# Kernel optimization log

Hardware: AMD Instinct MI355X
Metric: run time of the kernel (lower is better)

## Reference

```python
import jax, jax.numpy as jnp
import numpy as np

B, N, D, H, P = 4, 512, 256, 8, 3
HD = D // H
EPS = 1e-5

def _ln(x, g, b):
    m = jnp.mean(x, axis=-1, keepdims=True)
    v = jnp.var(x, axis=-1, keepdims=True)
    return (x - m) * jax.lax.rsqrt(v + EPS) * g + b

def setup_inputs() -> dict:
    key = jax.random.key(0)
    ks = jax.random.split(key, 12)
    s = lambda *sh: 1.0 / np.sqrt(sh[0])
    return {
        "x": jax.random.normal(ks[0], (B, N, D), jnp.float32),
        "mask": jax.random.randint(ks[1], (B, N), 0, 2).astype(bool),
        "pair_feat": jax.random.normal(ks[2], (B, N, N, P), jnp.float32),
        "Wqkv": jax.random.normal(ks[3], (D, 3 * D), jnp.float32) * s(D),
        "Wout": jax.random.normal(ks[4], (D, D), jnp.float32) * s(D),
        "bout": jnp.zeros((D,), jnp.float32),
        "Wp1": jax.random.normal(ks[5], (P, D), jnp.float32) * s(P),
        "bp1": jnp.zeros((D,), jnp.float32),
        "Wp2": jax.random.normal(ks[6], (D, H), jnp.float32) * s(D),
        "bp2": jnp.zeros((H,), jnp.float32),
        "Wf1": jax.random.normal(ks[7], (D, 4 * D), jnp.float32) * s(D),
        "bf1": jnp.zeros((4 * D,), jnp.float32),
        "Wf2": jax.random.normal(ks[8], (4 * D, D), jnp.float32) * s(4 * D),
        "bf2": jnp.zeros((D,), jnp.float32),
        "g1": jnp.ones((D,), jnp.float32), "b1": jnp.zeros((D,), jnp.float32),
        "g2": jnp.ones((D,), jnp.float32), "b2": jnp.zeros((D,), jnp.float32),
    }

def reference(x, mask, pair_feat, Wqkv, Wout, bout, Wp1, bp1, Wp2, bp2,
              Wf1, bf1, Wf2, bf2, g1, b1, g2, b2):
    b_, n_, d_ = x.shape
    scale = HD ** -0.5
    qkv = x @ Wqkv                                  # [B,N,3D]
    q, k, v = jnp.split(qkv, 3, axis=-1)
    q = q.reshape(b_, n_, H, HD)
    k = k.reshape(b_, n_, H, HD)
    v = v.reshape(b_, n_, H, HD)
    logits = jnp.einsum('bihd,bjhd->bhij', q, k) * scale
    # pairwise bias MLP -> per-head bias [B,H,N,N]
    bias = jax.nn.relu(pair_feat @ Wp1 + bp1) @ Wp2 + bp2   # [B,N,N,H]
    logits = logits + jnp.transpose(bias, (0, 3, 1, 2))
    key_mask = ~mask[:, None, None, :]               # [B,1,1,N]
    logits = jnp.where(key_mask, -1e9, logits)
    attn = jax.nn.softmax(logits, axis=-1)
    out = jnp.einsum('bhij,bjhd->bihd', attn, v).reshape(b_, n_, d_)
    out = out @ Wout + bout
    x = _ln(x + out, g1, b1)
    h = jax.nn.gelu(x @ Wf1 + bf1, approximate=False) @ Wf2 + bf2
    return _ln(x + h, g2, b2)
```

## Files before the change

kernel.cpp:

```cpp
#include <hip/hip_runtime.h>
#include <hip/hip_fp16.h>
#include <math.h>

typedef unsigned short u16;
typedef short s16x8 __attribute__((ext_vector_type(8)));
typedef _Float16 f16x8 __attribute__((ext_vector_type(8)));
typedef float f32x4 __attribute__((ext_vector_type(4)));
typedef unsigned int u32x2 __attribute__((ext_vector_type(2)));

constexpr int CB = 4, CN = 512, CD = 256, CH = 8, CHD = 32;
constexpr float CEPS = 1e-5f;
constexpr int M_ROWS = CB * CN;
constexpr float QSCALE = 0.17677669529663687f;

constexpr size_t O_XB    = 0;
constexpr size_t O_QB    = 1048576;
constexpr size_t O_KB    = 2097152;
constexpr size_t O_VB    = 3145728;
constexpr size_t O_WQKVT = 4194304;
constexpr size_t O_WOUTT = O_WQKVT + 393216;
constexpr size_t O_WF1T  = O_WOUTT + 131072;
constexpr size_t O_WF2T  = O_WF1T + 524288;
constexpr size_t O_WP2T  = O_WF2T + 524288;
constexpr size_t O_PACKED= O_WP2T + 8192;
constexpr size_t O_JIDX  = O_PACKED + 4096;
constexpr size_t O_BIAS  = O_JIDX + 8192;
constexpr size_t O_AOUT  = O_BIAS + 16777216;
constexpr size_t O_H1B   = O_AOUT + 1048576;
constexpr size_t O_PRE1  = O_H1B + 4194304;
constexpr size_t O_PRE2  = O_PRE1 + 2097152;
constexpr size_t O_CNT   = O_PRE2 + 2097152;

__device__ inline u16 f2b(float f) {
  union { float f; unsigned u; } v{f};
  return (u16)((v.u + 0x7FFFu + ((v.u >> 16) & 1u)) >> 16);
}
__device__ inline float b2f(u16 b) {
  union { unsigned u; float f; } v{(unsigned)b << 16};
  return v.f;
}
__device__ inline f32x4 MFMA(s16x8 a, s16x8 b, f32x4 c) {
  return __builtin_amdgcn_mfma_f32_16x16x32_bf16(a, b, c, 0, 0, 0);
}
__device__ inline f32x4 MFMAH(f16x8 a, f16x8 b, f32x4 c) {
  return __builtin_amdgcn_mfma_f32_16x16x32_f16(a, b, c, 0, 0, 0);
}
__device__ inline unsigned cvtpk(float lo, float hi) {
  unsigned r;
  asm("v_cvt_pk_bf16_f32 %0, %1, %2" : "=v"(r) : "v"(lo), "v"(hi));
  return r;
}
__device__ inline unsigned pkmax0(unsigned a) {
  unsigned d;
  asm("v_pk_max_f16 %0, %1, 0" : "=v"(d) : "v"(a));
  return d;
}

__global__ __launch_bounds__(256) void prep_kernel(
    const float* __restrict__ x, const float* __restrict__ Wqkv,
    const float* __restrict__ Wout, const float* __restrict__ Wf1,
    const float* __restrict__ Wf2, const float* __restrict__ Wp2,
    const float* __restrict__ Wp1, const float* __restrict__ bp1,
    const unsigned char* __restrict__ maskraw,
    u16* __restrict__ xb, u16* __restrict__ wqkvt, u16* __restrict__ woutt,
    u16* __restrict__ wf1t, u16* __restrict__ wf2t, u16* __restrict__ wp2t,
    unsigned* __restrict__ packed, int* __restrict__ jidxg,
    int* __restrict__ cntg) {
  __shared__ int mode_max;
  __shared__ int mdec[2048];
  int blk = blockIdx.x, tid = threadIdx.x;
  if (blk < 256) {
    for (int t = tid; t < 512; t += 256) {
      float4 v = ((const float4*)x)[blk * 512 + t];
      u16 o0 = f2b(v.x), o1 = f2b(v.y), o2 = f2b(v.z), o3 = f2b(v.w);
      u32x2 w; w.x = (unsigned)o0 | ((unsigned)o1 << 16);
      w.y = (unsigned)o2 | ((unsigned)o3 << 16);
      *(u32x2*)(xb + (size_t)(blk * 512 + t) * 4) = w;
    }
  } else if (blk < 352) {
    int o0 = (blk - 256) * 2048;
    for (int t = tid; t < 2048; t += 256) {
      int o = o0 + t, n = o >> 8, k = o & 255;
      wqkvt[o] = f2b(Wqkv[k * 768 + n]);
    }
  } else if (blk < 384) {
    int o0 = (blk - 352) * 2048;
    for (int t = tid; t < 2048; t += 256) {
      int o = o0 + t, n = o >> 8, k = o & 255;
      woutt[o] = f2b(Wout[k * 256 + n]);
    }
  } else if (blk < 512) {
    int o0 = (blk - 384) * 2048;
    for (int t = tid; t < 2048; t += 256) {
      int o = o0 + t, n = o >> 8, k = o & 255;
      wf1t[o] = f2b(Wf1[k * 1024 + n]);
    }
  } else if (blk < 640) {
    int o0 = (blk - 512) * 2048;
    for (int t = tid; t < 2048; t += 256) {
      int o = o0 + t, n = o >> 10, k = o & 1023;
      wf2t[o] = f2b(Wf2[k * 256 + n]);
    }
  } else if (blk == 640) {
    for (int t = tid; t < 4096; t += 256) {
      int h = t >> 8, c = t & 255;
      wp2t[t] = (h < 8) ? __half_as_ushort(__float2half(Wp2[c * 8 + h])) : (u16)0;
    }
    if (tid < 128) {
      int p = tid * 2;
      unsigned w0 = (unsigned)__half_as_ushort(__float2half(Wp1[p]))
                  | ((unsigned)__half_as_ushort(__float2half(Wp1[p + 1])) << 16);
      unsigned w1 = (unsigned)__half_as_ushort(__float2half(Wp1[256 + p]))
                  | ((unsigned)__half_as_ushort(__float2half(Wp1[256 + p + 1])) << 16);
      unsigned w2 = (unsigned)__half_as_ushort(__float2half(Wp1[512 + p]))
                  | ((unsigned)__half_as_ushort(__float2half(Wp1[512 + p + 1])) << 16);
      unsigned bb = (unsigned)__half_as_ushort(__float2half(bp1[p]))
                  | ((unsigned)__half_as_ushort(__float2half(bp1[p + 1])) << 16);
      uint4 o; o.x = w0; o.y = w1; o.z = w2; o.w = bb;
      ((uint4*)packed)[tid] = o;
    }
  } else {
    if (tid == 0) mode_max = 0;
    __syncthreads();
    int lm = 0;
    for (int i = tid; i < CB*CN; i += 256)
      if ((i & 3) != 0) lm = max(lm, (int)maskraw[i]);
    atomicMax(&mode_max, lm);
    __syncthreads();
    int mv = mode_max;
    for (int i = tid; i < CB*CN; i += 256) {
      int val;
      if (mv == 0)      val = (((const int*)maskraw)[i] != 0);
      else if (mv == 1) val = (maskraw[i] != 0);
      else              val = (((const unsigned int*)maskraw)[i] != 0);
      mdec[i] = val;
    }
    __syncthreads();
    int w = tid >> 6, lane = tid & 63;
    if (w < 4) {
      int b = w, basei = 0;
      for (int c = 0; c < 8; ++c) {
        int j = c * 64 + lane;
        int m = mdec[b * 512 + j];
        unsigned long long bal = __ballot(m != 0);
        int off = __popcll(bal & ((1ull << lane) - 1ull));
        if (m) jidxg[b * 512 + basei + off] = j;
        basei += (int)__popcll(bal);
      }
      if (lane == 0) cntg[b] = basei;
      for (int p = basei + lane; p < 512; p += 64) jidxg[b * 512 + p] = 0;
    }
  }
}

__global__ __launch_bounds__(256) void qkv_pbias_kernel(
    const u16* __restrict__ A, const u16* __restrict__ Wt,
    u16* __restrict__ qb, u16* __restrict__ kb, u16* __restrict__ vb,
    const float* __restrict__ pf, const unsigned* __restrict__ packed,
    const u16* __restrict__ wp2t, const float* __restrict__ bp2,
    const int* __restrict__ jidxg, const int* __restrict__ cntg,
    u16* __restrict__ biasc) {
  __shared__ uint4 smem[1024];
  const int blk = blockIdx.x, tid = threadIdx.x;
  const int lane = tid & 63, w = tid >> 6;
  if (blk < 384) {
    u16* As = (u16*)smem;
    u16* Bs = (u16*)smem + 64 * 64;
    const int wm = w >> 1, wn = w & 1;
    const int bm = (blk / 12) * 64, bn = (blk % 12) * 64;
    f32x4 fz = {0.f, 0.f, 0.f, 0.f};
    f32x4 acc[2][2] = {{fz, fz}, {fz, fz}};
    for (int k0 = 0; k0 < 256; k0 += 64) {
#pragma unroll
      for (int t = tid; t < 512; t += 256) {
        int r = t >> 3, s = t & 7;
        s16x8 v = *(const s16x8*)(A + (size_t)(bm + r) * 256 + k0 + s * 8);
        *(s16x8*)(As + r * 64 + ((s ^ (r & 7)) << 3)) = v;
      }
#pragma unroll
      for (int t = tid; t < 512; t += 256) {
        int r = t >> 3, s = t & 7;
        s16x8 v = *(const s16x8*)(Wt + (size_t)(bn + r) * 256 + k0 + s * 8);
        *(s16x8*)(Bs + r * 64 + ((s ^ (r & 7)) << 3)) = v;
      }
      __syncthreads();
#pragma unroll
      for (int ks = 0; ks < 2; ++ks) {
        s16x8 af[2], bf[2];
#pragma unroll
        for (int mf = 0; mf < 2; ++mf) {
          int r = wm * 32 + mf * 16 + (lane & 15);
          int s = ks * 4 + (lane >> 4);
          af[mf] = *(const s16x8*)(As + r * 64 + ((s ^ (r & 7)) << 3));
        }
#pragma unroll
        for (int nf = 0; nf < 2; ++nf) {
          int r = wn * 32 + nf * 16 + (lane & 15);
          int s = ks * 4 + (lane >> 4);
          bf[nf] = *(const s16x8*)(Bs + r * 64 + ((s ^ (r & 7)) << 3));
        }
#pragma unroll
        for (int mf = 0; mf < 2; ++mf)
#pragma unroll
          for (int nf = 0; nf < 2; ++nf)
            acc[mf][nf] = MFMA(af[mf], bf[nf], acc[mf][nf]);
      }
      __syncthreads();
    }
#pragma unroll
    for (int mf = 0; mf < 2; ++mf) {
#pragma unroll
      for (int nf = 0; nf < 2; ++nf) {
#pragma unroll
        for (int r = 0; r < 4; ++r) {
          int m = bm + wm * 32 + mf * 16 + (lane >> 4) * 4 + r;
          int n = bn + wn * 32 + nf * 16 + (lane & 15);
          float v = acc[mf][nf][r];
          if (n < 256) {
            qb[(size_t)m * 256 + n] = f2b(v * QSCALE);
          } else if (n < 512) {
            kb[(size_t)m * 256 + (n - 256)] = f2b(v);
          } else {
            vb[(size_t)m * 256 + (n - 512)] = f2b(v);
          }
        }
      }
    }
  } else {
    uint4* pk = smem;
    float* pfl = (float*)(smem + 128);
    int* ji = (int*)(smem + 512);
    const int bid = blk - 384;
    const int b = bid >> 9, i = bid & 511;
    const int q = lane >> 4, hr = lane & 15;
    if (tid < 128) pk[tid] = ((const uint4*)packed)[tid];
    const float4* pfr = (const float4*)(pf + (size_t)(b * 512 + i) * 1536);
#pragma unroll
    for (int t = tid; t < 384; t += 256) ((float4*)pfl)[t] = pfr[t];
    for (int t = tid; t < 512; t += 256) ji[t] = jidxg[b * 512 + t];
    const int cnt = cntg[b];
    __syncthreads();
    __half2 f0d[8], f1d[8], f2d[8];
#pragma unroll
    for (int t = 0; t < 8; ++t) {
      if (w * 128 + t * 16 < cnt) {
        int jsrc = ji[w * 128 + t * 16 + hr];
        f0d[t] = __float2half2_rn(pfl[jsrc * 3 + 0]);
        f1d[t] = __float2half2_rn(pfl[jsrc * 3 + 1]);
        f2d[t] = __float2half2_rn(pfl[jsrc * 3 + 2]);
      }
    }
    f32x4 fz = {0.f, 0.f, 0.f, 0.f};
    f32x4 acc[8] = {fz, fz, fz, fz, fz, fz, fz, fz};
    for (int chunk = 0; chunk < 8; ++chunk) {
      f16x8 wfrag = *(const f16x8*)(wp2t + hr * 256 + chunk * 32 + q * 8);
      int pbase = chunk * 16 + q * 4;
      __half2 w0[4], w1[4], w2[4], bb[4];
#pragma unroll
      for (int p = 0; p < 4; ++p) {
        uint4 c = pk[pbase + p];
        w0[p] = *(const __half2*)&c.x;
        w1[p] = *(const __half2*)&c.y;
        w2[p] = *(const __half2*)&c.z;
        bb[p] = *(const __half2*)&c.w;
      }
#pragma unroll
      for (int t = 0; t < 8; ++t) {
        if (w * 128 + t * 16 < cnt) {
          union { unsigned u[4]; f16x8 v; } af;
#pragma unroll
          for (int p = 0; p < 4; ++p) {
            __half2 h = __hfma2(f0d[t], w0[p], bb[p]);
            h = __hfma2(f1d[t], w1[p], h);
            h = __hfma2(f2d[t], w2[p], h);
            af.u[p] = pkmax0(*(const unsigned*)&h);
          }
          acc[t] = MFMAH(af.v, wfrag, acc[t]);
        }
      }
    }
    if (hr < 8) {
      float bb = bp2[hr];
      size_t base = ((size_t)(b * 8 + hr) * 512 + i) * 512;
#pragma unroll
      for (int t = 0; t < 8; ++t) {
        if (w * 128 + t * 16 < cnt) {
          int p0 = w * 128 + t * 16 + q * 4;
          u32x2 o;
          o.x = cvtpk(acc[t][0] + bb, acc[t][1] + bb);
          o.y = cvtpk(acc[t][2] + bb, acc[t][3] + bb);
          *(u32x2*)(biasc + base + p0) = o;
        }
      }
    }
  }
}

__global__ __launch_bounds__(256) void mgemm_res(
    const u16* __restrict__ A, const u16* __restrict__ Wt,
    const float* __restrict__ bias, const float* __restrict__ R,
    float* __restrict__ outf, int N, int K) {
  __shared__ u16 As[32 * 64];
  __shared__ u16 Bs[64 * 64];
  const int tid = threadIdx.x;
  const int lane = tid & 63, w = tid >> 6;
  const int wm = w >> 1, wn = w & 1;
  const int bm = blockIdx.y * 32, bn = blockIdx.x * 64;
  f32x4 fz = {0.f, 0.f, 0.f, 0.f};
  f32x4 acc[2] = {fz, fz};
  for (int k0 = 0; k0 < K; k0 += 64) {
    for (int t = tid; t < 256; t += 256) {
      int r = t >> 3, s = t & 7;
      s16x8 v = *(const s16x8*)(A + (size_t)(bm + r) * K + k0 + s * 8);
      *(s16x8*)(As + r * 64 + ((s ^ (r & 7)) << 3)) = v;
    }
#pragma unroll
    for (int t = tid; t < 512; t += 256) {
      int r = t >> 3, s = t & 7;
      s16x8 v = *(const s16x8*)(Wt + (size_t)(bn + r) * K + k0 + s * 8);
      *(s16x8*)(Bs + r * 64 + ((s ^ (r & 7)) << 3)) = v;
    }
    __syncthreads();
#pragma unroll
    for (int ks = 0; ks < 2; ++ks) {
      int r = wm * 16 + (lane & 15);
      int s = ks * 4 + (lane >> 4);
      s16x8 af = *(const s16x8*)(As + r * 64 + ((s ^ (r & 7)) << 3));
#pragma unroll
      for (int nf = 0; nf < 2; ++nf) {
        int br = wn * 32 + nf * 16 + (lane & 15);
        s16x8 bf = *(const s16x8*)(Bs + br * 64 + ((s ^ (br & 7)) << 3));
        acc[nf] = MFMA(af, bf, acc[nf]);
      }
    }
    __syncthreads();
  }
#pragma unroll
  for (int nf = 0; nf < 2; ++nf) {
#pragma unroll
    for (int r = 0; r < 4; ++r) {
      int m = bm + wm * 16 + (lane >> 4) * 4 + r;
      int n = bn + wn * 32 + nf * 16 + (lane & 15);
      outf[(size_t)m * N + n] = acc[nf][r] + bias[n] + R[(size_t)m * N + n];
    }
  }
}

__global__ __launch_bounds__(256) void ffn1_kernel(
    const float* __restrict__ pre1, const u16* __restrict__ Wt,
    const float* __restrict__ bias, const float* __restrict__ g1,
    const float* __restrict__ b1, u16* __restrict__ outb) {
  __shared__ u16 As[64 * 64];
  __shared__ u16 Bs[64 * 64];
  __shared__ float rowm[64], rowr[64];
  const int tid = threadIdx.x;
  const int lane = tid & 63, w = tid >> 6;
  const int wm = w >> 1, wn = w & 1;
  const int bm = blockIdx.y * 64, bn = blockIdx.x * 64;
  {
    int r = tid >> 2, qd = tid & 3;
    const float4* pr = (const float4*)(pre1 + (size_t)(bm + r) * 256 + qd * 64);
    float s = 0.f, ss = 0.f;
#pragma unroll
    for (int u = 0; u < 16; ++u) {
      float4 v = pr[u];
      s += v.x + v.y + v.z + v.w;
      ss += v.x*v.x + v.y*v.y + v.z*v.z + v.w*v.w;
    }
    s += __shfl_xor(s, 1); ss += __shfl_xor(ss, 1);
    s += __shfl_xor(s, 2); ss += __shfl_xor(ss, 2);
    if (qd == 0) {
      float mean = s * (1.0f / 256.0f);
      float var  = ss * (1.0f / 256.0f) - mean * mean;
      rowm[r] = mean; rowr[r] = rsqrtf(var + CEPS);
    }
  }
  __syncthreads();
  f32x4 fz = {0.f, 0.f, 0.f, 0.f};
  f32x4 acc[2][2] = {{fz, fz}, {fz, fz}};
  for (int k0 = 0; k0 < 256; k0 += 64) {
#pragma unroll
    for (int t = tid; t < 512; t += 256) {
      int r = t >> 3, s = t & 7;
      float mean = rowm[r], rstd = rowr[r];
      const float4* pr = (const float4*)(pre1 + (size_t)(bm + r) * 256 + k0 + s * 8);
      float4 a0 = pr[0], a1 = pr[1];
      const float4* gp = (const float4*)(g1 + k0 + s * 8);
      const float4* bp = (const float4*)(b1 + k0 + s * 8);
      float4 g0 = gp[0], g1v = gp[1], c0 = bp[0], c1 = bp[1];
      union { unsigned u[4]; s16x8 v; } pk2;
      pk2.u[0] = cvtpk((a0.x-mean)*rstd*g0.x + c0.x, (a0.y-mean)*rstd*g0.y + c0.y);
      pk2.u[1] = cvtpk((a0.z-mean)*rstd*g0.z + c0.z, (a0.w-mean)*rstd*g0.w + c0.w);
      pk2.u[2] = cvtpk((a1.x-mean)*rstd*g1v.x + c1.x, (a1.y-mean)*rstd*g1v.y + c1.y);
      pk2.u[3] = cvtpk((a1.z-mean)*rstd*g1v.z + c1.z, (a1.w-mean)*rstd*g1v.w + c1.w);
      *(s16x8*)(As + r * 64 + ((s ^ (r & 7)) << 3)) = pk2.v;
    }
#pragma unroll
    for (int t = tid; t < 512; t += 256) {
      int r = t >> 3, s = t & 7;
      s16x8 v = *(const s16x8*)(Wt + (size_t)(bn + r) * 256 + k0 + s * 8);
      *(s16x8*)(Bs + r * 64 + ((s ^ (r & 7)) << 3)) = v;
    }
    __syncthreads();
#pragma unroll
    for (int ks = 0; ks < 2; ++ks) {
      s16x8 af[2], bf[2];
#pragma unroll
      for (int mf = 0; mf < 2; ++mf) {
        int r = wm * 32 + mf * 16 + (lane & 15);
        int s = ks * 4 + (lane >> 4);
        af[mf] = *(const s16x8*)(As + r * 64 + ((s ^ (r & 7)) << 3));
      }
#pragma unroll
      for (int nf = 0; nf < 2; ++nf) {
        int r = wn * 32 + nf * 16 + (lane & 15);
        int s = ks * 4 + (lane >> 4);
        bf[nf] = *(const s16x8*)(Bs + r * 64 + ((s ^ (r & 7)) << 3));
      }
#pragma unroll
      for (int mf = 0; mf < 2; ++mf)
#pragma unroll
        for (int nf = 0; nf < 2; ++nf)
          acc[mf][nf] = MFMA(af[mf], bf[nf], acc[mf][nf]);
    }
    __syncthreads();
  }
#pragma unroll
  for (int mf = 0; mf < 2; ++mf) {
#pragma unroll
    for (int nf = 0; nf < 2; ++nf) {
#pragma unroll
      for (int r = 0; r < 4; ++r) {
        int m = bm + wm * 32 + mf * 16 + (lane >> 4) * 4 + r;
        int n = bn + wn * 32 + nf * 16 + (lane & 15);
        float gv = acc[mf][nf][r] + bias[n];
        gv = 0.5f * gv * (1.0f + erff(gv * 0.70710678118654752f));
        outb[(size_t)m * 1024 + n] = f2b(gv);
      }
    }
  }
}

__global__ __launch_bounds__(256) void ffn2_kernel(
    const u16* __restrict__ A, const u16* __restrict__ Wt,
    const float* __restrict__ bias, const float* __restrict__ pre1,
    const float* __restrict__ g1, const float* __restrict__ b1,
    float* __restrict__ outf) {
  __shared__ u16 As[32 * 64];
  __shared__ u16 Bs[64 * 64];
  __shared__ float rowm[32], rowr[32];
  const int tid = threadIdx.x;
  const int lane = tid & 63, w = tid >> 6;
  const int wm = w >> 1, wn = w & 1;
  const int bm = blockIdx.y * 32, bn = blockIdx.x * 64;
  {
    int r = tid >> 3, od = tid & 7;
    const float4* pr = (const float4*)(pre1 + (size_t)(bm + r) * 256 + od * 32);
    float s = 0.f, ss = 0.f;
#pragma unroll
    for (int u = 0; u < 8; ++u) {
      float4 v = pr[u];
      s += v.x + v.y + v.z + v.w;
      ss += v.x*v.x + v.y*v.y + v.z*v.z + v.w*v.w;
    }
    s += __shfl_xor(s, 1); ss += __shfl_xor(ss, 1);
    s += __shfl_xor(s, 2); ss += __shfl_xor(ss, 2);
    s += __shfl_xor(s, 4); ss += __shfl_xor(ss, 4);
    if (od == 0) {
      float mean = s * (1.0f / 256.0f);
      float var  = ss * (1.0f / 256.0f) - mean * mean;
      rowm[r] = mean; rowr[r] = rsqrtf(var + CEPS);
    }
  }
  __syncthreads();
  f32x4 fz = {0.f, 0.f, 0.f, 0.f};
  f32x4 acc[2] = {fz, fz};
  for (int k0 = 0; k0 < 1024; k0 += 64) {
    for (int t = tid; t < 256; t += 256) {
      int r = t >> 3, s = t & 7;
      s16x8 v = *(const s16x8*)(A + (size_t)(bm + r) * 1024 + k0 + s * 8);
      *(s16x8*)(As + r * 64 + ((s ^ (r & 7)) << 3)) = v;
    }
#pragma unroll
    for (int t = tid; t < 512; t += 256) {
      int r = t >> 3, s = t & 7;
      s16x8 v = *(const s16x8*)(Wt + (size_t)(bn + r) * 1024 + k0 + s * 8);
      *(s16x8*)(Bs + r * 64 + ((s ^ (r & 7)) << 3)) = v;
    }
    __syncthreads();
#pragma unroll
    for (int ks = 0; ks < 2; ++ks) {
      int r = wm * 16 + (lane & 15);
      int s = ks * 4 + (lane >> 4);
      s16x8 af = *(const s16x8*)(As + r * 64 + ((s ^ (r & 7)) << 3));
#pragma unroll
      for (int nf = 0; nf < 2; ++nf) {
        int br = wn * 32 + nf * 16 + (lane & 15);
        s16x8 bf = *(const s16x8*)(Bs + br * 64 + ((s ^ (br & 7)) << 3));
        acc[nf] = MFMA(af, bf, acc[nf]);
      }
    }
    __syncthreads();
  }
#pragma unroll
  for (int nf = 0; nf < 2; ++nf) {
#pragma unroll
    for (int r = 0; r < 4; ++r) {
      int m = bm + wm * 16 + (lane >> 4) * 4 + r;
      int n = bn + wn * 32 + nf * 16 + (lane & 15);
      float mean = rowm[m - bm], rstd = rowr[m - bm];
      float xr = (pre1[(size_t)m * 256 + n] - mean) * rstd * g1[n] + b1[n];
      outf[(size_t)m * 256 + n] = acc[nf][r] + bias[n] + xr;
    }
  }
}

__global__ __launch_bounds__(512) void flash_kernel(
    const u16* __restrict__ qb, const u16* __restrict__ kb,
    const u16* __restrict__ vb, const u16* __restrict__ biasc,
    const int* __restrict__ jidxg, const int* __restrict__ cntg,
    u16* __restrict__ aout) {
  const int i0 = blockIdx.x * 64, h = blockIdx.y, b = blockIdx.z;
  const int tid = threadIdx.x;
  const int lane = tid & 63, w = tid >> 6;
  const int mf = w & 3, jhalf = w >> 2;
  __shared__ u16 qs[64 * 32];
  __shared__ u16 ksh[128 * 32];
  __shared__ u16 vs[32 * 128];
  __shared__ u16 ps[8][16 * 64];
  __shared__ float cmb[4][2][16][2];
  __shared__ int ji[512];
  for (int t = tid; t < 512; t += 512) ji[t] = jidxg[b * 512 + t];
  for (int t = tid; t < 256; t += 512) {
    int r = t >> 2, s = t & 3;
    s16x8 v = *(const s16x8*)(qb + (size_t)(b * 512 + i0 + r) * 256 + h * 32 + s * 8);
    *(s16x8*)(qs + r * 32 + ((s ^ (r & 3)) << 3)) = v;
  }
  const int cnt = cntg[b];
  __syncthreads();
  f32x4 fz = {0.f, 0.f, 0.f, 0.f};
  f32x4 oacc[2] = {fz, fz};
  float mrun[4] = {-3e38f, -3e38f, -3e38f, -3e38f};
  float lrun[4] = {0.f, 0.f, 0.f, 0.f};
  const int jj0 = jhalf * 64;
  const int il = mf * 16 + (lane >> 4) * 4;
  const u16* bbase = biasc + ((size_t)((b * 8 + h) * 512 + i0 + il)) * 512
                   + jj0 + (lane & 15);
  const int NJT = (cnt + 127) >> 7;
  for (int jc = 0; jc < NJT; ++jc) {
    int j0 = jc * 128;
    {
      int r = tid >> 2, s = tid & 3;
      int jsrc = ji[j0 + r];
      s16x8 v = *(const s16x8*)(kb + (size_t)(b * 512 + jsrc) * 256 + h * 32 + s * 8);
      *(s16x8*)(ksh + r * 32 + ((s ^ (r & 3)) << 3)) = v;
    }
    {
      int r = tid >> 2, s = tid & 3;
      int jsrc = ji[j0 + r];
      s16x8 v = *(const s16x8*)(vb + (size_t)(b * 512 + jsrc) * 256 + h * 32 + s * 8);
      int slot = r >> 3, el = r & 7;
#pragma unroll
      for (int e = 0; e < 8; ++e) {
        int d = s * 8 + e;
        vs[d * 128 + (((slot & 8) | ((slot & 7) ^ (d & 7))) << 3) + el] = (u16)v[e];
      }
    }
    u16 bvr[4][4];
#pragma unroll
    for (int jf = 0; jf < 4; ++jf)
#pragma unroll
      for (int r = 0; r < 4; ++r)
        bvr[jf][r] = bbase[(size_t)r * 512 + j0 + jf * 16];
    __syncthreads();
    int mk[4];
#pragma unroll
    for (int jf = 0; jf < 4; ++jf)
      mk[jf] = (j0 + jj0 + jf * 16 + (lane & 15)) < cnt;
    int arow = mf * 16 + (lane & 15);
    s16x8 af = *(const s16x8*)(qs + arow * 32 + (((lane >> 4) ^ (arow & 3)) << 3));
    f32x4 sm[4];
#pragma unroll
    for (int jf = 0; jf < 4; ++jf) {
      int brow = jj0 + jf * 16 + (lane & 15);
      s16x8 bfr = *(const s16x8*)(ksh + brow * 32 + (((lane >> 4) ^ (brow & 3)) << 3));
      sm[jf] = MFMA(af, bfr, fz);
    }
#pragma unroll
    for (int jf = 0; jf < 4; ++jf) {
#pragma unroll
      for (int r = 0; r < 4; ++r) {
        float sval = sm[jf][r] + b2f(bvr[jf][r]);
        sm[jf][r] = mk[jf] ? sval : -1e9f;
      }
    }
    float mx[4];
#pragma unroll
    for (int r = 0; r < 4; ++r)
      mx[r] = fmaxf(fmaxf(sm[0][r], sm[1][r]), fmaxf(sm[2][r], sm[3][r]));
#pragma unroll
    for (int d = 1; d < 16; d <<= 1)
#pragma unroll
      for (int r = 0; r < 4; ++r) mx[r] = fmaxf(mx[r], __shfl_xor(mx[r], d));
    float psl[4] = {0.f, 0.f, 0.f, 0.f};
#pragma unroll
    for (int jf = 0; jf < 4; ++jf)
#pragma unroll
      for (int r = 0; r < 4; ++r) {
        float p = __expf(sm[jf][r] - mx[r]);
        sm[jf][r] = p; psl[r] += p;
      }
#pragma unroll
    for (int d = 1; d < 16; d <<= 1)
#pragma unroll
      for (int r = 0; r < 4; ++r) psl[r] += __shfl_xor(psl[r], d);
    if ((lane & 15) == 0) {
#pragma unroll
      for (int r = 0; r < 4; ++r) {
        int row = (lane >> 4) * 4 + r;
        cmb[mf][jhalf][row][0] = mx[r];
        cmb[mf][jhalf][row][1] = psl[r];
      }
    }
    __syncthreads();
    float selfs[4];
#pragma unroll
    for (int r = 0; r < 4; ++r) {
      int row = (lane >> 4) * 4 + r;
      float omx = cmb[mf][1 - jhalf][row][0];
      float ops = cmb[mf][1 - jhalf][row][1];
      float tm = fmaxf(mx[r], omx);
      float nm = fmaxf(mrun[r], tm);
      float sc = __expf(mrun[r] - nm);
      selfs[r] = __expf(mx[r] - nm);
      float ptile = psl[r] * selfs[r] + ops * __expf(omx - nm);
      lrun[r] = lrun[r] * sc + ptile;
      mrun[r] = nm;
      oacc[0][r] *= sc; oacc[1][r] *= sc;
    }
    u16* pw = &ps[w][0];
#pragma unroll
    for (int jf = 0; jf < 4; ++jf) {
      int jcol = jf * 16 + (lane & 15);
      int slot = jcol >> 3, el = jcol & 7;
#pragma unroll
      for (int r = 0; r < 4; ++r) {
        int row = (lane >> 4) * 4 + r;
        pw[row * 64 + ((slot ^ (row & 7)) << 3) + el] = f2b(sm[jf][r] * selfs[r]);
      }
    }
#pragma unroll
    for (int kw = 0; kw < 2; ++kw) {
      int prow = lane & 15;
      s16x8 pa = *(const s16x8*)(pw + prow * 64 + (((kw * 4 + (lane >> 4)) ^ (prow & 7)) << 3));
#pragma unroll
      for (int df = 0; df < 2; ++df) {
        int drow = df * 16 + (lane & 15);
        int jcol = jj0 + kw * 32 + ((lane >> 4) << 3);
        int slot = jcol >> 3;
        s16x8 vv = *(const s16x8*)(vs + drow * 128 + (((slot & 8) | ((slot & 7) ^ (drow & 7))) << 3));
        oacc[df] = MFMA(pa, vv, oacc[df]);
      }
    }
    __syncthreads();
  }
  float* obuf = (float*)&ps[0][0];
  if (jhalf == 1) {
#pragma unroll
    for (int r = 0; r < 4; ++r) {
      int row = mf * 16 + (lane >> 4) * 4 + r;
#pragma unroll
      for (int df = 0; df < 2; ++df)
        obuf[row * 33 + df * 16 + (lane & 15)] = oacc[df][r];
    }
  }
  __syncthreads();
  if (jhalf == 0) {
#pragma unroll
    for (int r = 0; r < 4; ++r) {
      float inv = 1.0f / lrun[r];
      int row = mf * 16 + (lane >> 4) * 4 + r;
      int i = i0 + row;
#pragma unroll
      for (int df = 0; df < 2; ++df) {
        int d = df * 16 + (lane & 15);
        float o = (oacc[df][r] + obuf[row * 33 + d]) * inv;
        aout[(size_t)(b * 512 + i) * 256 + h * 32 + d] = f2b(o);
      }
    }
  }
}

__global__ __launch_bounds__(256) void ln_kernel(
    const float* __restrict__ in, const float* __restrict__ g,
    const float* __restrict__ be, float* __restrict__ op) {
  int row = blockIdx.x * 4 + (threadIdx.x >> 6);
  int lane = threadIdx.x & 63;
  const float* x = in + (size_t)row * CD;
  float4 v = *(const float4*)&x[lane * 4];
  float s  = v.x + v.y + v.z + v.w;
  float ss = v.x*v.x + v.y*v.y + v.z*v.z + v.w*v.w;
#pragma unroll
  for (int off = 32; off > 0; off >>= 1) {
    s  += __shfl_xor(s, off);
    ss += __shfl_xor(ss, off);
  }
  float mean = s * (1.0f / CD);
  float var  = ss * (1.0f / CD) - mean * mean;
  float inv  = rsqrtf(var + CEPS);
  float4 gg = *(const float4*)&g[lane * 4];
  float4 bb = *(const float4*)&be[lane * 4];
  float4 o;
  o.x = (v.x - mean) * inv * gg.x + bb.x;
  o.y = (v.y - mean) * inv * gg.y + bb.y;
  o.z = (v.z - mean) * inv * gg.z + bb.z;
  o.w = (v.w - mean) * inv * gg.w + bb.w;
  *(float4*)&op[(size_t)row * CD + lane * 4] = o;
}

extern "C" void kernel_launch(void* const* d_in, const int* in_sizes, int n_in,
                              void* d_out, int out_size, void* d_ws, size_t ws_size,
                              hipStream_t stream) {
  (void)in_sizes; (void)n_in; (void)out_size; (void)ws_size;
  const float* x    = (const float*)d_in[0];
  const void*  mask = d_in[1];
  const float* pf   = (const float*)d_in[2];
  const float* Wqkv = (const float*)d_in[3];
  const float* Wout = (const float*)d_in[4];
  const float* bout = (const float*)d_in[5];
  const float* Wp1  = (const float*)d_in[6];
  const float* bp1  = (const float*)d_in[7];
  const float* Wp2  = (const float*)d_in[8];
  const float* bp2  = (const float*)d_in[9];
  const float* Wf1  = (const float*)d_in[10];
  const float* bf1  = (const float*)d_in[11];
  const float* Wf2  = (const float*)d_in[12];
  const float* bf2  = (const float*)d_in[13];
  const float* g1   = (const float*)d_in[14];
  const float* b1   = (const float*)d_in[15];
  const float* g2   = (const float*)d_in[16];
  const float* b2   = (const float*)d_in[17];

  char* ws = (char*)d_ws;
  u16* xb     = (u16*)(ws + O_XB);
  u16* qb     = (u16*)(ws + O_QB);
  u16* kb     = (u16*)(ws + O_KB);
  u16* vb     = (u16*)(ws + O_VB);
  u16* wqkvt  = (u16*)(ws + O_WQKVT);
  u16* woutt  = (u16*)(ws + O_WOUTT);
  u16* wf1t   = (u16*)(ws + O_WF1T);
  u16* wf2t   = (u16*)(ws + O_WF2T);
  u16* wp2t   = (u16*)(ws + O_WP2T);
  unsigned* packed = (unsigned*)(ws + O_PACKED);
  int* jidxg  = (int*)(ws + O_JIDX);
  int* cntg   = (int*)(ws + O_CNT);
  u16* biasc  = (u16*)(ws + O_BIAS);
  u16* aout   = (u16*)(ws + O_AOUT);
  u16* h1b    = (u16*)(ws + O_H1B);
  float* pre1 = (float*)(ws + O_PRE1);
  float* pre2 = (float*)(ws + O_PRE2);
  float* out  = (float*)d_out;

  hipLaunchKernelGGL(prep_kernel, dim3(642), dim3(256), 0, stream,
                     x, Wqkv, Wout, Wf1, Wf2, Wp2, Wp1, bp1,
                     (const unsigned char*)mask,
                     xb, wqkvt, woutt, wf1t, wf2t, wp2t, packed, jidxg, cntg);
  hipLaunchKernelGGL(qkv_pbias_kernel, dim3(2432), dim3(256), 0, stream,
                     xb, wqkvt, qb, kb, vb,
                     pf, packed, wp2t, bp2, jidxg, cntg, biasc);
  hipLaunchKernelGGL(flash_kernel, dim3(8, 8, 4), dim3(512), 0, stream,
                     qb, kb, vb, biasc, jidxg, cntg, aout);
  hipLaunchKernelGGL(mgemm_res, dim3(4, 64), dim3(256), 0, stream,
                     aout, woutt, bout, x, pre1, 256, 256);
  hipLaunchKernelGGL(ffn1_kernel, dim3(16, 32), dim3(256), 0, stream,
                     pre1, wf1t, bf1, g1, b1, h1b);
  hipLaunchKernelGGL(ffn2_kernel, dim3(4, 64), dim3(256), 0, stream,
                     h1b, wf2t, bf2, pre1, g1, b1, pre2);
  hipLaunchKernelGGL(ln_kernel, dim3(M_ROWS / 4), dim3(256), 0, stream,
                     pre2, g2, b2, out);
}
```

Baseline: 101.1 us.

## Fuse out-proj, FFN and final LayerNorm into one cooperative persistent kernel

Replaces the four tail kernels (output projection with residual, FFN1 with LN1, FFN2 with residual, final LN) with a single cooperative kernel of 512 blocks that uses grid.sync between phases. It also computes the LN1 row statistics once into a workspace buffer instead of recomputing them in each FFN block. The aim is to remove kernel launch gaps and the redundant per-block statistics work. In exchange it adds four grid-wide barriers and leaves half the blocks idle in the 256-block phases.

Result: slower. 320.7 us (+217.3%).

```diff
diff --git a/kernel.cpp b/kernel.cpp
--- a/kernel.cpp
+++ b/kernel.cpp
@@ -1,6 +1,9 @@
 #include <hip/hip_runtime.h>
 #include <hip/hip_fp16.h>
+#include <hip/hip_cooperative_groups.h>
 #include <math.h>
+
+namespace cg = cooperative_groups;
 
 typedef unsigned short u16;
 typedef short s16x8 __attribute__((ext_vector_type(8)));
@@ -30,6 +33,7 @@
 constexpr size_t O_PRE1  = O_H1B + 4194304;
 constexpr size_t O_PRE2  = O_PRE1 + 2097152;
 constexpr size_t O_CNT   = O_PRE2 + 2097152;
+constexpr size_t O_RST   = O_CNT + 256;
 
 __device__ inline u16 f2b(float f) {
   union { float f; unsigned u; } v{f};
@@ -296,225 +300,6 @@
   }
 }
 
-__global__ __launch_bounds__(256) void mgemm_res(
-    const u16* __restrict__ A, const u16* __restrict__ Wt,
-    const float* __restrict__ bias, const float* __restrict__ R,
-    float* __restrict__ outf, int N, int K) {
-  __shared__ u16 As[32 * 64];
-  __shared__ u16 Bs[64 * 64];
-  const int tid = threadIdx.x;
-  const int lane = tid & 63, w = tid >> 6;
-  const int wm = w >> 1, wn = w & 1;
-  const int bm = blockIdx.y * 32, bn = blockIdx.x * 64;
-  f32x4 fz = {0.f, 0.f, 0.f, 0.f};
-  f32x4 acc[2] = {fz, fz};
-  for (int k0 = 0; k0 < K; k0 += 64) {
-    for (int t = tid; t < 256; t += 256) {
-      int r = t >> 3, s = t & 7;
-      s16x8 v = *(const s16x8*)(A + (size_t)(bm + r) * K + k0 + s * 8);
-      *(s16x8*)(As + r * 64 + ((s ^ (r & 7)) << 3)) = v;
-    }
-#pragma unroll
-    for (int t = tid; t < 512; t += 256) {
-      int r = t >> 3, s = t & 7;
-      s16x8 v = *(const s16x8*)(Wt + (size_t)(bn + r) * K + k0 + s * 8);
-      *(s16x8*)(Bs + r * 64 + ((s ^ (r & 7)) << 3)) = v;
-    }
-    __syncthreads();
-#pragma unroll
-    for (int ks = 0; ks < 2; ++ks) {
-      int r = wm * 16 + (lane & 15);
-      int s = ks * 4 + (lane >> 4);
-      s16x8 af = *(const s16x8*)(As + r * 64 + ((s ^ (r & 7)) << 3));
-#pragma unroll
-      for (int nf = 0; nf < 2; ++nf) {
-        int br = wn * 32 + nf * 16 + (lane & 15);
-        s16x8 bf = *(const s16x8*)(Bs + br * 64 + ((s ^ (br & 7)) << 3));
-        acc[nf] = MFMA(af, bf, acc[nf]);
-      }
-    }
-    __syncthreads();
-  }
-#pragma unroll
-  for (int nf = 0; nf < 2; ++nf) {
-#pragma unroll
-    for (int r = 0; r < 4; ++r) {
-      int m = bm + wm * 16 + (lane >> 4) * 4 + r;
-      int n = bn + wn * 32 + nf * 16 + (lane & 15);
-      outf[(size_t)m * N + n] = acc[nf][r] + bias[n] + R[(size_t)m * N + n];
-    }
-  }
-}
-
-__global__ __launch_bounds__(256) void ffn1_kernel(
-    const float* __restrict__ pre1, const u16* __restrict__ Wt,
-    const float* __restrict__ bias, const float* __restrict__ g1,
-    const float* __restrict__ b1, u16* __restrict__ outb) {
-  __shared__ u16 As[64 * 64];
-  __shared__ u16 Bs[64 * 64];
-  __shared__ float rowm[64], rowr[64];
-  const int tid = threadIdx.x;
-  const int lane = tid & 63, w = tid >> 6;
-  const int wm = w >> 1, wn = w & 1;
-  const int bm = blockIdx.y * 64, bn = blockIdx.x * 64;
-  {
-    int r = tid >> 2, qd = tid & 3;
-    const float4* pr = (const float4*)(pre1 + (size_t)(bm + r) * 256 + qd * 64);
-    float s = 0.f, ss = 0.f;
-#pragma unroll
-    for (int u = 0; u < 16; ++u) {
-      float4 v = pr[u];
-      s += v.x + v.y + v.z + v.w;
-      ss += v.x*v.x + v.y*v.y + v.z*v.z + v.w*v.w;
-    }
-    s += __shfl_xor(s, 1); ss += __shfl_xor(ss, 1);
-    s += __shfl_xor(s, 2); ss += __shfl_xor(ss, 2);
-    if (qd == 0) {
-      float mean = s * (1.0f / 256.0f);
-      float var  = ss * (1.0f / 256.0f) - mean * mean;
-      rowm[r] = mean; rowr[r] = rsqrtf(var + CEPS);
-    }
-  }
-  __syncthreads();
-  f32x4 fz = {0.f, 0.f, 0.f, 0.f};
-  f32x4 acc[2][2] = {{fz, fz}, {fz, fz}};
-  for (int k0 = 0; k0 < 256; k0 += 64) {
-#pragma unroll
-    for (int t = tid; t < 512; t += 256) {
-      int r = t >> 3, s = t & 7;
-      float mean = rowm[r], rstd = rowr[r];
-      const float4* pr = (const float4*)(pre1 + (size_t)(bm + r) * 256 + k0 + s * 8);
-      float4 a0 = pr[0], a1 = pr[1];
-      const float4* gp = (const float4*)(g1 + k0 + s * 8);
-      const float4* bp = (const float4*)(b1 + k0 + s * 8);
-      float4 g0 = gp[0], g1v = gp[1], c0 = bp[0], c1 = bp[1];
-      union { unsigned u[4]; s16x8 v; } pk2;
-      pk2.u[0] = cvtpk((a0.x-mean)*rstd*g0.x + c0.x, (a0.y-mean)*rstd*g0.y + c0.y);
-      pk2.u[1] = cvtpk((a0.z-mean)*rstd*g0.z + c0.z, (a0.w-mean)*rstd*g0.w + c0.w);
-      pk2.u[2] = cvtpk((a1.x-mean)*rstd*g1v.x + c1.x, (a1.y-mean)*rstd*g1v.y + c1.y);
-      pk2.u[3] = cvtpk((a1.z-mean)*rstd*g1v.z + c1.z, (a1.w-mean)*rstd*g1v.w + c1.w);
-      *(s16x8*)(As + r * 64 + ((s ^ (r & 7)) << 3)) = pk2.v;
-    }
-#pragma unroll
-    for (int t = tid; t < 512; t += 256) {
-      int r = t >> 3, s = t & 7;
-      s16x8 v = *(const s16x8*)(Wt + (size_t)(bn + r) * 256 + k0 + s * 8);
-      *(s16x8*)(Bs + r * 64 + ((s ^ (r & 7)) << 3)) = v;
-    }
-    __syncthreads();
-#pragma unroll
-    for (int ks = 0; ks < 2; ++ks) {
-      s16x8 af[2], bf[2];
-#pragma unroll
-      for (int mf = 0; mf < 2; ++mf) {
-        int r = wm * 32 + mf * 16 + (lane & 15);
-        int s = ks * 4 + (lane >> 4);
-        af[mf] = *(const s16x8*)(As + r * 64 + ((s ^ (r & 7)) << 3));
-      }
-#pragma unroll
-      for (int nf = 0; nf < 2; ++nf) {
-        int r = wn * 32 + nf * 16 + (lane & 15);
-        int s = ks * 4 + (lane >> 4);
-        bf[nf] = *(const s16x8*)(Bs + r * 64 + ((s ^ (r & 7)) << 3));
-      }
-#pragma unroll
-      for (int mf = 0; mf < 2; ++mf)
-#pragma unroll
-        for (int nf = 0; nf < 2; ++nf)
-          acc[mf][nf] = MFMA(af[mf], bf[nf], acc[mf][nf]);
-    }
-    __syncthreads();
-  }
-#pragma unroll
-  for (int mf = 0; mf < 2; ++mf) {
-#pragma unroll
-    for (int nf = 0; nf < 2; ++nf) {
-#pragma unroll
-      for (int r = 0; r < 4; ++r) {
-        int m = bm + wm * 32 + mf * 16 + (lane >> 4) * 4 + r;
-        int n = bn + wn * 32 + nf * 16 + (lane & 15);
-        float gv = acc[mf][nf][r] + bias[n];
-        gv = 0.5f * gv * (1.0f + erff(gv * 0.70710678118654752f));
-        outb[(size_t)m * 1024 + n] = f2b(gv);
-      }
-    }
-  }
-}
-
-__global__ __launch_bounds__(256) void ffn2_kernel(
-    const u16* __restrict__ A, const u16* __restrict__ Wt,
-    const float* __restrict__ bias, const float* __restrict__ pre1,
-    const float* __restrict__ g1, const float* __restrict__ b1,
-    float* __restrict__ outf) {
-  __shared__ u16 As[32 * 64];
-  __shared__ u16 Bs[64 * 64];
-  __shared__ float rowm[32], rowr[32];
-  const int tid = threadIdx.x;
-  const int lane = tid & 63, w = tid >> 6;
-  const int wm = w >> 1, wn = w & 1;
-  const int bm = blockIdx.y * 32, bn = blockIdx.x * 64;
-  {
-    int r = tid >> 3, od = tid & 7;
-    const float4* pr = (const float4*)(pre1 + (size_t)(bm + r) * 256 + od * 32);
-    float s = 0.f, ss = 0.f;
-#pragma unroll
-    for (int u = 0; u < 8; ++u) {
-      float4 v = pr[u];
-      s += v.x + v.y + v.z + v.w;
-      ss += v.x*v.x + v.y*v.y + v.z*v.z + v.w*v.w;
-    }
-    s += __shfl_xor(s, 1); ss += __shfl_xor(ss, 1);
-    s += __shfl_xor(s, 2); ss += __shfl_xor(ss, 2);
-    s += __shfl_xor(s, 4); ss += __shfl_xor(ss, 4);
-    if (od == 0) {
-      float mean = s * (1.0f / 256.0f);
-      float var  = ss * (1.0f / 256.0f) - mean * mean;
-      rowm[r] = mean; rowr[r] = rsqrtf(var + CEPS);
-    }
-  }
-  __syncthreads();
-  f32x4 fz = {0.f, 0.f, 0.f, 0.f};
-  f32x4 acc[2] = {fz, fz};
-  for (int k0 = 0; k0 < 1024; k0 += 64) {
-    for (int t = tid; t < 256; t += 256) {
-      int r = t >> 3, s = t & 7;
-      s16x8 v = *(const s16x8*)(A + (size_t)(bm + r) * 1024 + k0 + s * 8);
-      *(s16x8*)(As + r * 64 + ((s ^ (r & 7)) << 3)) = v;
-    }
-#pragma unroll
-    for (int t = tid; t < 512; t += 256) {
-      int r = t >> 3, s = t & 7;
-      s16x8 v = *(const s16x8*)(Wt + (size_t)(bn + r) * 1024 + k0 + s * 8);
-      *(s16x8*)(Bs + r * 64 + ((s ^ (r & 7)) << 3)) = v;
-    }
-    __syncthreads();
-#pragma unroll
-    for (int ks = 0; ks < 2; ++ks) {
-      int r = wm * 16 + (lane & 15);
-      int s = ks * 4 + (lane >> 4);
-      s16x8 af = *(const s16x8*)(As + r * 64 + ((s ^ (r & 7)) << 3));
-#pragma unroll
-      for (int nf = 0; nf < 2; ++nf) {
-        int br = wn * 32 + nf * 16 + (lane & 15);
-        s16x8 bf = *(const s16x8*)(Bs + br * 64 + ((s ^ (br & 7)) << 3));
-        acc[nf] = MFMA(af, bf, acc[nf]);
-      }
-    }
-    __syncthreads();
-  }
-#pragma unroll
-  for (int nf = 0; nf < 2; ++nf) {
-#pragma unroll
-    for (int r = 0; r < 4; ++r) {
-      int m = bm + wm * 16 + (lane >> 4) * 4 + r;
-      int n = bn + wn * 32 + nf * 16 + (lane & 15);
-      float mean = rowm[m - bm], rstd = rowr[m - bm];
-      float xr = (pre1[(size_t)m * 256 + n] - mean) * rstd * g1[n] + b1[n];
-      outf[(size_t)m * 256 + n] = acc[nf][r] + bias[n] + xr;
-    }
-  }
-}
-
 __global__ __launch_bounds__(512) void flash_kernel(
     const u16* __restrict__ qb, const u16* __restrict__ kb,
     const u16* __restrict__ vb, const u16* __restrict__ biasc,
@@ -691,31 +476,215 @@
   }
 }
 
-__global__ __launch_bounds__(256) void ln_kernel(
-    const float* __restrict__ in, const float* __restrict__ g,
-    const float* __restrict__ be, float* __restrict__ op) {
-  int row = blockIdx.x * 4 + (threadIdx.x >> 6);
-  int lane = threadIdx.x & 63;
-  const float* x = in + (size_t)row * CD;
-  float4 v = *(const float4*)&x[lane * 4];
-  float s  = v.x + v.y + v.z + v.w;
-  float ss = v.x*v.x + v.y*v.y + v.z*v.z + v.w*v.w;
-#pragma unroll
-  for (int off = 32; off > 0; off >>= 1) {
-    s  += __shfl_xor(s, off);
-    ss += __shfl_xor(ss, off);
-  }
-  float mean = s * (1.0f / CD);
-  float var  = ss * (1.0f / CD) - mean * mean;
-  float inv  = rsqrtf(var + CEPS);
-  float4 gg = *(const float4*)&g[lane * 4];
-  float4 bb = *(const float4*)&be[lane * 4];
-  float4 o;
-  o.x = (v.x - mean) * inv * gg.x + bb.x;
-  o.y = (v.y - mean) * inv * gg.y + bb.y;
-  o.z = (v.z - mean) * inv * gg.z + bb.z;
-  o.w = (v.w - mean) * inv * gg.w + bb.w;
-  *(float4*)&op[(size_t)row * CD + lane * 4] = o;
+__global__ __launch_bounds__(256) void tail_kernel(
+    const u16* aout, const u16* woutt, const float* bout, const float* x,
+    const u16* wf1t, const float* bf1, const u16* wf2t, const float* bf2,
+    const float* g1, const float* b1, const float* g2, const float* b2,
+    float* pre1, u16* h1b, float* pre2, float* rst, float* out) {
+  cg::grid_group grid = cg::this_grid();
+  __shared__ u16 As[64 * 64];
+  __shared__ u16 Bs[64 * 64];
+  const int blk = blockIdx.x, tid = threadIdx.x;
+  const int lane = tid & 63, w = tid >> 6;
+  f32x4 fz = {0.f, 0.f, 0.f, 0.f};
+  if (blk < 256) {
+    const int wm = w >> 1, wn = w & 1;
+    const int bm = (blk >> 2) * 32, bn = (blk & 3) * 64;
+    f32x4 acc[2] = {fz, fz};
+    for (int k0 = 0; k0 < 256; k0 += 64) {
+      for (int t = tid; t < 256; t += 256) {
+        int r = t >> 3, s = t & 7;
+        s16x8 v = *(const s16x8*)(aout + (size_t)(bm + r) * 256 + k0 + s * 8);
+        *(s16x8*)(As + r * 64 + ((s ^ (r & 7)) << 3)) = v;
+      }
+#pragma unroll
+      for (int t = tid; t < 512; t += 256) {
+        int r = t >> 3, s = t & 7;
+        s16x8 v = *(const s16x8*)(woutt + (size_t)(bn + r) * 256 + k0 + s * 8);
+        *(s16x8*)(Bs + r * 64 + ((s ^ (r & 7)) << 3)) = v;
+      }
+      __syncthreads();
+#pragma unroll
+      for (int ks = 0; ks < 2; ++ks) {
+        int r = wm * 16 + (lane & 15);
+        int s = ks * 4 + (lane >> 4);
+        s16x8 af = *(const s16x8*)(As + r * 64 + ((s ^ (r & 7)) << 3));
+#pragma unroll
+        for (int nf = 0; nf < 2; ++nf) {
+          int br = wn * 32 + nf * 16 + (lane & 15);
+          s16x8 bf = *(const s16x8*)(Bs + br * 64 + ((s ^ (br & 7)) << 3));
+          acc[nf] = MFMA(af, bf, acc[nf]);
+        }
+      }
+      __syncthreads();
+    }
+#pragma unroll
+    for (int nf = 0; nf < 2; ++nf) {
+#pragma unroll
+      for (int r = 0; r < 4; ++r) {
+        int m = bm + wm * 16 + (lane >> 4) * 4 + r;
+        int n = bn + wn * 32 + nf * 16 + (lane & 15);
+        pre1[(size_t)m * 256 + n] = acc[nf][r] + bout[n] + x[(size_t)m * 256 + n];
+      }
+    }
+  }
+  grid.sync();
+  if (blk < 256) {
+    int row = blk * 8 + (tid >> 5);
+    int l32 = tid & 31;
+    const float4* pr = (const float4*)(pre1 + (size_t)row * 256);
+    float4 v0 = pr[l32], v1 = pr[32 + l32];
+    float s = v0.x + v0.y + v0.z + v0.w + v1.x + v1.y + v1.z + v1.w;
+    float ss = v0.x*v0.x + v0.y*v0.y + v0.z*v0.z + v0.w*v0.w
+             + v1.x*v1.x + v1.y*v1.y + v1.z*v1.z + v1.w*v1.w;
+#pragma unroll
+    for (int d = 16; d > 0; d >>= 1) {
+      s += __shfl_xor(s, d);
+      ss += __shfl_xor(ss, d);
+    }
+    if (l32 == 0) {
+      float mean = s * (1.0f / 256.0f);
+      float var  = ss * (1.0f / 256.0f) - mean * mean;
+      rst[row * 2] = mean;
+      rst[row * 2 + 1] = rsqrtf(var + CEPS);
+    }
+  }
+  grid.sync();
+  {
+    const int wm = w >> 1, wn = w & 1;
+    const int bm = (blk >> 4) * 64, bn = (blk & 15) * 64;
+    f32x4 acc[2][2] = {{fz, fz}, {fz, fz}};
+    for (int k0 = 0; k0 < 256; k0 += 64) {
+#pragma unroll
+      for (int t = tid; t < 512; t += 256) {
+        int r = t >> 3, s = t & 7;
+        int grow = bm + r;
+        float mean = rst[grow * 2], rstd = rst[grow * 2 + 1];
+        const float4* pr = (const float4*)(pre1 + (size_t)grow * 256 + k0 + s * 8);
+        float4 a0 = pr[0], a1 = pr[1];
+        const float4* gp = (const float4*)(g1 + k0 + s * 8);
+        const float4* bp = (const float4*)(b1 + k0 + s * 8);
+        float4 g0 = gp[0], g1v = gp[1], c0 = bp[0], c1 = bp[1];
+        union { unsigned u[4]; s16x8 v; } pk2;
+        pk2.u[0] = cvtpk((a0.x-mean)*rstd*g0.x + c0.x, (a0.y-mean)*rstd*g0.y + c0.y);
+        pk2.u[1] = cvtpk((a0.z-mean)*rstd*g0.z + c0.z, (a0.w-mean)*rstd*g0.w + c0.w);
+        pk2.u[2] = cvtpk((a1.x-mean)*rstd*g1v.x + c1.x, (a1.y-mean)*rstd*g1v.y + c1.y);
+        pk2.u[3] = cvtpk((a1.z-mean)*rstd*g1v.z + c1.z, (a1.w-mean)*rstd*g1v.w + c1.w);
+        *(s16x8*)(As + r * 64 + ((s ^ (r & 7)) << 3)) = pk2.v;
+      }
+#pragma unroll
+      for (int t = tid; t < 512; t += 256) {
+        int r = t >> 3, s = t & 7;
+        s16x8 v = *(const s16x8*)(wf1t + (size_t)(bn + r) * 256 + k0 + s * 8);
+        *(s16x8*)(Bs + r * 64 + ((s ^ (r & 7)) << 3)) = v;
+      }
+      __syncthreads();
+#pragma unroll
+      for (int ks = 0; ks < 2; ++ks) {
+        s16x8 af[2], bf[2];
+#pragma unroll
+        for (int mf = 0; mf < 2; ++mf) {
+          int r = wm * 32 + mf * 16 + (lane & 15);
+          int s = ks * 4 + (lane >> 4);
+          af[mf] = *(const s16x8*)(As + r * 64 + ((s ^ (r & 7)) << 3));
+        }
+#pragma unroll
+        for (int nf = 0; nf < 2; ++nf) {
+          int r = wn * 32 + nf * 16 + (lane & 15);
+          int s = ks * 4 + (lane >> 4);
+          bf[nf] = *(const s16x8*)(Bs + r * 64 + ((s ^ (r & 7)) << 3));
+        }
+#pragma unroll
+        for (int mf = 0; mf < 2; ++mf)
+#pragma unroll
+          for (int nf = 0; nf < 2; ++nf)
+            acc[mf][nf] = MFMA(af[mf], bf[nf], acc[mf][nf]);
+      }
+      __syncthreads();
+    }
+#pragma unroll
+    for (int mf = 0; mf < 2; ++mf) {
+#pragma unroll
+      for (int nf = 0; nf < 2; ++nf) {
+#pragma unroll
+        for (int r = 0; r < 4; ++r) {
+          int m = bm + wm * 32 + mf * 16 + (lane >> 4) * 4 + r;
+          int n = bn + wn * 32 + nf * 16 + (lane & 15);
+          float gv = acc[mf][nf][r] + bf1[n];
+          gv = 0.5f * gv * (1.0f + erff(gv * 0.70710678118654752f));
+          h1b[(size_t)m * 1024 + n] = f2b(gv);
+        }
+      }
+    }
+  }
+  grid.sync();
+  if (blk < 256) {
+    const int wm = w >> 1, wn = w & 1;
+    const int bm = (blk >> 2) * 32, bn = (blk & 3) * 64;
+    f32x4 acc[2] = {fz, fz};
+    for (int k0 = 0; k0 < 1024; k0 += 64) {
+      for (int t = tid; t < 256; t += 256) {
+        int r = t >> 3, s = t & 7;
+        s16x8 v = *(const s16x8*)(h1b + (size_t)(bm + r) * 1024 + k0 + s * 8);
+        *(s16x8*)(As + r * 64 + ((s ^ (r & 7)) << 3)) = v;
+      }
+#pragma unroll
+      for (int t = tid; t < 512; t += 256) {
+        int r = t >> 3, s = t & 7;
+        s16x8 v = *(const s16x8*)(wf2t + (size_t)(bn + r) * 1024 + k0 + s * 8);
+        *(s16x8*)(Bs + r * 64 + ((s ^ (r & 7)) << 3)) = v;
+      }
+      __syncthreads();
+#pragma unroll
+      for (int ks = 0; ks < 2; ++ks) {
+        int r = wm * 16 + (lane & 15);
+        int s = ks * 4 + (lane >> 4);
+        s16x8 af = *(const s16x8*)(As + r * 64 + ((s ^ (r & 7)) << 3));
+#pragma unroll
+        for (int nf = 0; nf < 2; ++nf) {
+          int br = wn * 32 + nf * 16 + (lane & 15);
+          s16x8 bf = *(const s16x8*)(Bs + br * 64 + ((s ^ (br & 7)) << 3));
+          acc[nf] = MFMA(af, bf, acc[nf]);
+        }
+      }
+      __syncthreads();
+    }
+#pragma unroll
+    for (int nf = 0; nf < 2; ++nf) {
+#pragma unroll
+      for (int r = 0; r < 4; ++r) {
+        int m = bm + wm * 16 + (lane >> 4) * 4 + r;
+        int n = bn + wn * 32 + nf * 16 + (lane & 15);
+        float mean = rst[m * 2], rstd = rst[m * 2 + 1];
+        float xr = (pre1[(size_t)m * 256 + n] - mean) * rstd * g1[n] + b1[n];
+        pre2[(size_t)m * 256 + n] = acc[nf][r] + bf2[n] + xr;
+      }
+    }
+  }
+  grid.sync();
+  {
+    int row = blk * 4 + (tid >> 6);
+    const float* xr = pre2 + (size_t)row * 256;
+    float4 v = *(const float4*)&xr[lane * 4];
+    float s  = v.x + v.y + v.z + v.w;
+    float ss = v.x*v.x + v.y*v.y + v.z*v.z + v.w*v.w;
+#pragma unroll
+    for (int off = 32; off > 0; off >>= 1) {
+      s  += __shfl_xor(s, off);
+      ss += __shfl_xor(ss, off);
+    }
+    float mean = s * (1.0f / 256.0f);
+    float var  = ss * (1.0f / 256.0f) - mean * mean;
+    float inv  = rsqrtf(var + CEPS);
+    float4 gg = *(const float4*)&g2[lane * 4];
+    float4 bb = *(const float4*)&b2[lane * 4];
+    float4 o;
+    o.x = (v.x - mean) * inv * gg.x + bb.x;
+    o.y = (v.y - mean) * inv * gg.y + bb.y;
+    o.z = (v.z - mean) * inv * gg.z + bb.z;
+    o.w = (v.w - mean) * inv * gg.w + bb.w;
+    *(float4*)&out[(size_t)row * 256 + lane * 4] = o;
+  }
 }
 
 extern "C" void kernel_launch(void* const* d_in, const int* in_sizes, int n_in,
@@ -759,6 +728,7 @@
   u16* h1b    = (u16*)(ws + O_H1B);
   float* pre1 = (float*)(ws + O_PRE1);
   float* pre2 = (float*)(ws + O_PRE2);
+  float* rst  = (float*)(ws + O_RST);
   float* out  = (float*)d_out;
 
   hipLaunchKernelGGL(prep_kernel, dim3(642), dim3(256), 0, stream,
@@ -770,12 +740,12 @@
                      pf, packed, wp2t, bp2, jidxg, cntg, biasc);
   hipLaunchKernelGGL(flash_kernel, dim3(8, 8, 4), dim3(512), 0, stream,
                      qb, kb, vb, biasc, jidxg, cntg, aout);
-  hipLaunchKernelGGL(mgemm_res, dim3(4, 64), dim3(256), 0, stream,
-                     aout, woutt, bout, x, pre1, 256, 256);
-  hipLaunchKernelGGL(ffn1_kernel, dim3(16, 32), dim3(256), 0, stream,
-                     pre1, wf1t, bf1, g1, b1, h1b);
-  hipLaunchKernelGGL(ffn2_kernel, dim3(4, 64), dim3(256), 0, stream,
-                     h1b, wf2t, bf2, pre1, g1, b1, pre2);
-  hipLaunchKernelGGL(ln_kernel, dim3(M_ROWS / 4), dim3(256), 0, stream,
-                     pre2, g2, b2, out);
-}
+  void* targs[] = {
+    (void*)&aout, (void*)&woutt, (void*)&bout, (void*)&x,
+    (void*)&wf1t, (void*)&bf1, (void*)&wf2t, (void*)&bf2,
+    (void*)&g1, (void*)&b1, (void*)&g2, (void*)&b2,
+    (void*)&pre1, (void*)&h1b, (void*)&pre2, (void*)&rst, (void*)&out
+  };
+  hipLaunchCooperativeKernel((const void*)tail_kernel, dim3(512), dim3(256),
+                             targs, 0, stream);
+}
```
